# Kernel tuning notes

Hardware: AMD Instinct MI355X
Metric: run time of the kernel (lower is better)

Reference implementation:

```python
import jax, jax.numpy as jnp
import numpy as np

VOCAB, POS = 50000, 64
WDIM, PDIM = 256, 64
LSTM_H = 512          # total bidirectional width
H = LSTM_H // 2       # per-direction hidden
MLP = 512
SEQ = 512


def _lstm_dir(x, Wih, Whh, bih, bhh, reverse):
    # x: [T, in]; Wih: [4H, in]; Whh: [4H, H]; gate order i,f,g,o (PyTorch)
    Hd = Whh.shape[1]
    def step(carry, xt):
        h, c = carry
        g = xt @ Wih.T + bih + h @ Whh.T + bhh
        i, f, gg, o = jnp.split(g, 4, axis=-1)
        c = jax.nn.sigmoid(f) * c + jax.nn.sigmoid(i) * jnp.tanh(gg)
        h = jax.nn.sigmoid(o) * jnp.tanh(c)
        return (h, c), h
    xs = x[::-1] if reverse else x
    init = (jnp.zeros((Hd,), x.dtype), jnp.zeros((Hd,), x.dtype))
    _, hs = jax.lax.scan(step, init, xs)
    return hs[::-1] if reverse else hs


def _bilstm_layer(x, Wih, Whh, bih, bhh):
    # params stacked over direction: [2, ...]
    hf = _lstm_dir(x, Wih[0], Whh[0], bih[0], bhh[0], False)
    hb = _lstm_dir(x, Wih[1], Whh[1], bih[1], bhh[1], True)
    return jnp.concatenate([hf, hb], axis=-1)  # [T, 2H]


def setup_inputs() -> dict:
    key = jax.random.key(0)
    ks = jax.random.split(key, 16)
    s = 0.05
    inp = {
        "word_tensor": jax.random.randint(ks[0], (SEQ,), 0, VOCAB),
        "pos_tensor": jax.random.randint(ks[1], (SEQ,), 0, POS),
        "word_emb": jax.random.normal(ks[2], (VOCAB, WDIM), jnp.float32) * s,
        "pos_emb": jax.random.normal(ks[3], (POS, PDIM), jnp.float32) * s,
        # layer 0: input = WDIM+PDIM = 320
        "wih0": jax.random.normal(ks[4], (2, 4 * H, WDIM + PDIM), jnp.float32) * s,
        "whh0": jax.random.normal(ks[5], (2, 4 * H, H), jnp.float32) * s,
        "bih0": jax.random.normal(ks[6], (2, 4 * H), jnp.float32) * s,
        "bhh0": jax.random.normal(ks[7], (2, 4 * H), jnp.float32) * s,
        # layer 1: input = 2H = LSTM_H
        "wih1": jax.random.normal(ks[8], (2, 4 * H, LSTM_H), jnp.float32) * s,
        "whh1": jax.random.normal(ks[9], (2, 4 * H, H), jnp.float32) * s,
        "bih1": jax.random.normal(ks[10], (2, 4 * H), jnp.float32) * s,
        "bhh1": jax.random.normal(ks[11], (2, 4 * H), jnp.float32) * s,
        # pairwise MLP: Linear(2*LSTM_H -> MLP), output_layer(MLP -> 1)
        "W_lin": jax.random.normal(ks[12], (MLP, 2 * LSTM_H), jnp.float32) * s,
        "b_lin": jax.random.normal(ks[13], (MLP,), jnp.float32) * s,
        "w_out": jax.random.normal(ks[14], (1, MLP), jnp.float32) * s,
        "b_out": jax.random.normal(ks[15], (1,), jnp.float32) * s,
    }
    return inp


def reference(word_tensor, pos_tensor, word_emb, pos_emb,
              wih0, whh0, bih0, bhh0, wih1, whh1, bih1, bhh1,
              W_lin, b_lin, w_out, b_out):
    # embeddings: [T, 320]
    embeds = jnp.concatenate([word_emb[word_tensor], pos_emb[pos_tensor]], axis=-1)
    x = _bilstm_layer(embeds, wih0, whh0, bih0, bhh0)
    lstm_out = _bilstm_layer(x, wih1, whh1, bih1, bhh1)  # [T, LSTM_H]
    # Fused pairwise scoring: Linear(cat(h_h, h_m)) = h_h @ W1.T + h_m @ W2.T + b
    W1, W2 = W_lin[:, :LSTM_H], W_lin[:, LSTM_H:]
    u = lstm_out @ W1.T  # [T, MLP] head half
    v = lstm_out @ W2.T  # [T, MLP] modifier half
    neuron = jnp.tanh(u[:, None, :] + v[None, :, :] + b_lin)  # [T, T, MLP]
    score = neuron @ w_out[0] + b_out[0]                      # [T, T]
    n = score.shape[0]
    # original puts NaN on the diagonal (invalid h==m pairs); use 0.0 sentinel
    return jnp.where(jnp.eye(n, dtype=bool), 0.0, score)
```

## Files before the change

### kernel.cpp

```cpp
#include <hip/hip_runtime.h>
#include <cstddef>
#include <cstdint>

constexpr int kSeq = 512;
constexpr int kH   = 256;
constexpr int kG   = 1024;
constexpr int kE   = 320;
constexpr int kLH  = 512;
constexpr int kMLP = 512;

typedef _Float16 h2 __attribute__((ext_vector_type(2)));

__device__ __forceinline__ float fexp2f(float x) {
  float r; asm("v_exp_f32 %0, %1" : "=v"(r) : "v"(x)); return r;
}
__device__ __forceinline__ float frcpf(float x) {
  float r; asm("v_rcp_f32 %0, %1" : "=v"(r) : "v"(x)); return r;
}
__device__ __forceinline__ float sigm(float x) {
  return frcpf(1.0f + fexp2f(-1.4426950408889634f * x));
}
__device__ __forceinline__ float tanh_(float x) {
  return 1.0f - 2.0f * frcpf(1.0f + fexp2f(2.8853900817779268f * x));
}

__device__ __forceinline__ float fdot2(unsigned int w, unsigned int h, float c) {
#if __has_builtin(__builtin_amdgcn_fdot2)
  return __builtin_amdgcn_fdot2(__builtin_bit_cast(h2, w),
                                __builtin_bit_cast(h2, h), c, false);
#else
  const h2 wv = __builtin_bit_cast(h2, w);
  const h2 hv = __builtin_bit_cast(h2, h);
  return c + (float)wv.x * (float)hv.x + (float)wv.y * (float)hv.y;
#endif
}

__device__ __forceinline__ unsigned int packh2(float a, float b) {
  h2 v; v.x = (_Float16)a; v.y = (_Float16)b;
  return __builtin_bit_cast(unsigned int, v);
}

__global__ void embed_k(const int* __restrict__ wt, const int* __restrict__ pt,
                        const float* __restrict__ we, const float* __restrict__ pe,
                        float* __restrict__ X) {
  const int t = blockIdx.x;
  const int c = threadIdx.x;
  const int w = wt[t];
  const int p = pt[t];
  X[t * kE + c] = (c < 256) ? we[(size_t)w * 256 + c] : pe[p * 64 + (c - 256)];
}

__global__ __launch_bounds__(256) void pack_wh_k(
    const float* __restrict__ whh0, const float* __restrict__ whh1,
    unsigned int* __restrict__ wh16) {
  const int idx = blockIdx.x * 256 + threadIdx.x;
  const int layer = idx >> 18;
  const int li = idx & 262143;
  const int rowg = li >> 7;
  const int c2 = li & 127;
  const float* src = (layer ? whh1 : whh0) + (size_t)rowg * kH + c2 * 2;
  wh16[idx] = packh2(src[0], src[1]);
}

template <int BM, int BN, int BK>
__global__ __launch_bounds__(256) void gemm_nt(
    const float* __restrict__ A, int lda,
    const float* __restrict__ B, int ldb,
    const float* __restrict__ b1, const float* __restrict__ b2, float scale,
    float* __restrict__ C, int csm, int csn, int K) {
  const int tid = threadIdx.x;
  const int m0 = blockIdx.y * BM;
  const int n0 = blockIdx.x * BN;
  __shared__ float As[BK][BM];
  __shared__ float Bs[BK][BN];
  const int lm = tid >> 2;
  const int lk = tid & 3;
  const int tx = tid & 15;
  const int ty = tid >> 4;
  float acc[4][4] = {};
  for (int k0 = 0; k0 < K; k0 += BK) {
    const float4 av = *(const float4*)(A + (size_t)(m0 + lm) * lda + k0 + lk * 4);
    const float4 bv = *(const float4*)(B + (size_t)(n0 + lm) * ldb + k0 + lk * 4);
    __syncthreads();
    As[lk * 4 + 0][lm] = av.x; As[lk * 4 + 1][lm] = av.y;
    As[lk * 4 + 2][lm] = av.z; As[lk * 4 + 3][lm] = av.w;
    Bs[lk * 4 + 0][lm] = bv.x; Bs[lk * 4 + 1][lm] = bv.y;
    Bs[lk * 4 + 2][lm] = bv.z; Bs[lk * 4 + 3][lm] = bv.w;
    __syncthreads();
#pragma unroll
    for (int kk = 0; kk < BK; ++kk) {
      const float4 a = *(const float4*)&As[kk][ty * 4];
      const float4 b = *(const float4*)&Bs[kk][tx * 4];
      acc[0][0] = fmaf(a.x, b.x, acc[0][0]);
      acc[0][1] = fmaf(a.x, b.y, acc[0][1]);
      acc[0][2] = fmaf(a.x, b.z, acc[0][2]);
      acc[0][3] = fmaf(a.x, b.w, acc[0][3]);
      acc[1][0] = fmaf(a.y, b.x, acc[1][0]);
      acc[1][1] = fmaf(a.y, b.y, acc[1][1]);
      acc[1][2] = fmaf(a.y, b.z, acc[1][2]);
      acc[1][3] = fmaf(a.y, b.w, acc[1][3]);
      acc[2][0] = fmaf(a.z, b.x, acc[2][0]);
      acc[2][1] = fmaf(a.z, b.y, acc[2][1]);
      acc[2][2] = fmaf(a.z, b.z, acc[2][2]);
      acc[2][3] = fmaf(a.z, b.w, acc[2][3]);
      acc[3][0] = fmaf(a.w, b.x, acc[3][0]);
      acc[3][1] = fmaf(a.w, b.y, acc[3][1]);
      acc[3][2] = fmaf(a.w, b.z, acc[3][2]);
      acc[3][3] = fmaf(a.w, b.w, acc[3][3]);
    }
  }
#pragma unroll
  for (int ii = 0; ii < 4; ++ii) {
#pragma unroll
    for (int jj = 0; jj < 4; ++jj) {
      const int m = m0 + ty * 4 + ii;
      const int n = n0 + tx * 4 + jj;
      float v = acc[ii][jj];
      if (b1) v += b1[n];
      if (b2) v += b2[n];
      C[(size_t)m * csm + (size_t)n * csn] = v * scale;
    }
  }
}

__global__ __launch_bounds__(1024)
__attribute__((amdgpu_waves_per_eu(4, 4)))
void lstm_scan_2cu(
    const unsigned int* __restrict__ wh16,
    const float* __restrict__ pre,
    float* __restrict__ out,
    float* __restrict__ comm)
{
  const int bx = blockIdx.x;
  int d, s;
  if (bx == 0)      { d = 0; s = 0; }
  else if (bx == 1) { d = 1; s = 0; }
  else if (bx == 8) { d = 0; s = 1; }
  else if (bx == 9) { d = 1; s = 1; }
  else return;

  const int t = threadIdx.x;
  const int w = t >> 6;
  const int L = t & 63;
  const int ch = w & 1;
  const int r  = (w >> 1) * 64 + L;
  const int g  = r >> 7;
  const int j  = r & 127;
  const int grow = g * kH + s * 128 + j;

  uint4 wr[16];
  {
    const uint4* wp = (const uint4*)wh16 + ((size_t)d * kG + grow) * 32 + ch * 16;
#pragma unroll
    for (int k = 0; k < 16; ++k) wr[k] = wp[k];
  }

  __shared__ __align__(16) _Float16 hh16[kH];
  __shared__ float pbuf[2][512];
  if (t < 128) ((h2*)hh16)[t] = h2{(_Float16)0.f, (_Float16)0.f};
  float c = 0.0f;
  __syncthreads();

  const uint4* hh4 = (const uint4*)hh16;
  float* cm = comm + (size_t)d * kSeq * kH;
  const bool isGate = (t < 128);
  const bool isPoll = (t >= 512 && t < 640);
  const int re = (1 - s) * 128 + (t - 512);

  for (int u = 0; u < kSeq; ++u) {
    const int ts = d ? (kSeq - 1 - u) : u;
    float pg0 = 0.f, pg1 = 0.f, pg2 = 0.f, pg3 = 0.f;
    if (isGate) {
      const float* pp = pre + ((size_t)d * kSeq + ts) * kG + s * 128 + t;
      pg0 = pp[0]; pg1 = pp[256]; pg2 = pp[512]; pg3 = pp[768];
    }
    {
      const uint4* hp = hh4 + ch * 16;
      float a0 = 0.f, a1 = 0.f, a2 = 0.f, a3 = 0.f;
#pragma unroll
      for (int k = 0; k < 16; ++k) {
        const uint4 hv = hp[k];
        a0 = fdot2(wr[k].x, hv.x, a0);
        a1 = fdot2(wr[k].y, hv.y, a1);
        a2 = fdot2(wr[k].z, hv.z, a2);
        a3 = fdot2(wr[k].w, hv.w, a3);
      }
      pbuf[ch][r] = (a0 + a1) + (a2 + a3);
    }
    __syncthreads();

    if (isGate) {
      const float gi = pbuf[0][t]       + pbuf[1][t]       + pg0;
      const float gf = pbuf[0][128 + t] + pbuf[1][128 + t] + pg1;
      const float gg = pbuf[0][256 + t] + pbuf[1][256 + t] + pg2;
      const float go = pbuf[0][384 + t] + pbuf[1][384 + t] + pg3;
      const float iv = sigm(gi), fv = sigm(gf);
      const float gv = tanh_(gg), ov = sigm(go);
      c = fv * c + iv * gv;
      const float h = ov * tanh_(c);
      const int e = s * 128 + t;
      __hip_atomic_store(&cm[(size_t)u * kH + e], h + 2.0f,
                         __ATOMIC_RELAXED, __HIP_MEMORY_SCOPE_AGENT);
      hh16[e] = (_Float16)h;
      out[(size_t)ts * kLH + d * kH + e] = h;
    } else if (isPoll) {
      const float* src = &cm[(size_t)u * kH + re];
      float a = __hip_atomic_load(src, __ATOMIC_RELAXED, __HIP_MEMORY_SCOPE_AGENT);
      float b = __hip_atomic_load(src, __ATOMIC_RELAXED, __HIP_MEMORY_SCOPE_AGENT);
      while (a == 0.0f) {
        a = b;
        b = __hip_atomic_load(src, __ATOMIC_RELAXED, __HIP_MEMORY_SCOPE_AGENT);
      }
      hh16[re] = (_Float16)(a - 2.0f);
    }
    __syncthreads();
  }
}

__global__ __launch_bounds__(512) void score_k(
    const float* __restrict__ Up, const float* __restrict__ VT,
    const float* __restrict__ wout, const float* __restrict__ bout,
    float* __restrict__ out) {
  const int i = blockIdx.x;
  const int j = threadIdx.x;
  __shared__ float u_sh[kMLP];
  __shared__ float w_sh[kMLP];
  u_sh[j] = Up[(size_t)i * kMLP + j];
  w_sh[j] = wout[j];
  __syncthreads();
  float acc = 0.0f;
#pragma unroll 4
  for (int m = 0; m < kMLP; ++m) {
    const float x = u_sh[m] + VT[(size_t)m * kSeq + j];
    const float th = 1.0f - 2.0f * frcpf(1.0f + fexp2f(x));
    acc = fmaf(th, w_sh[m], acc);
  }
  const float s = acc + bout[0];
  out[(size_t)i * kSeq + j] = (j == i) ? 0.0f : s;
}

extern "C" void kernel_launch(void* const* d_in, const int* in_sizes, int n_in,
                              void* d_out, int out_size, void* d_ws, size_t ws_size,
                              hipStream_t stream) {
  const int*   wt   = (const int*)d_in[0];
  const int*   pt   = (const int*)d_in[1];
  const float* wemb = (const float*)d_in[2];
  const float* pemb = (const float*)d_in[3];
  const float* wih0 = (const float*)d_in[4];
  const float* whh0 = (const float*)d_in[5];
  const float* bih0 = (const float*)d_in[6];
  const float* bhh0 = (const float*)d_in[7];
  const float* wih1 = (const float*)d_in[8];
  const float* whh1 = (const float*)d_in[9];
  const float* bih1 = (const float*)d_in[10];
  const float* bhh1 = (const float*)d_in[11];
  const float* wlin = (const float*)d_in[12];
  const float* blin = (const float*)d_in[13];
  const float* wout = (const float*)d_in[14];
  const float* bout = (const float*)d_in[15];
  float* outp = (float*)d_out;

  float* ws   = (float*)d_ws;
  float* X    = ws;
  float* PG0  = X + kSeq * kE;
  float* X1   = PG0 + 2 * kSeq * kG;
  float* PG1  = X1 + kSeq * kLH;
  float* LOUT = PG1 + 2 * kSeq * kG;
  float* U    = LOUT + kSeq * kLH;
  float* VT   = U + kSeq * kMLP;
  float* COMM0 = VT + kSeq * kMLP;
  float* COMM1 = COMM0 + 2 * kSeq * kH;
  unsigned int* WH16 = (unsigned int*)(COMM1 + 2 * kSeq * kH);

  const float SC = 2.8853900817779268f;

  hipMemsetAsync(COMM0, 0, 2 * 2 * kSeq * kH * sizeof(float), stream);

  embed_k<<<kSeq, kE, 0, stream>>>(wt, pt, wemb, pemb, X);
  pack_wh_k<<<2048, 256, 0, stream>>>(whh0, whh1, WH16);

  for (int d = 0; d < 2; ++d) {
    gemm_nt<64, 64, 16><<<dim3(kG / 64, kSeq / 64), 256, 0, stream>>>(
        X, kE, wih0 + (size_t)d * kG * kE, kE,
        bih0 + d * kG, bhh0 + d * kG, 1.0f,
        PG0 + (size_t)d * kSeq * kG, kG, 1, kE);
  }
  lstm_scan_2cu<<<10, 1024, 0, stream>>>(WH16, PG0, X1, COMM0);

  for (int d = 0; d < 2; ++d) {
    gemm_nt<64, 64, 16><<<dim3(kG / 64, kSeq / 64), 256, 0, stream>>>(
        X1, kLH, wih1 + (size_t)d * kG * kLH, kLH,
        bih1 + d * kG, bhh1 + d * kG, 1.0f,
        PG1 + (size_t)d * kSeq * kG, kG, 1, kLH);
  }
  lstm_scan_2cu<<<10, 1024, 0, stream>>>(WH16 + 2 * kG * 128, PG1, LOUT, COMM1);

  gemm_nt<64, 64, 16><<<dim3(kMLP / 64, kSeq / 64), 256, 0, stream>>>(
      LOUT, kLH, wlin, 2 * kLH, nullptr, nullptr, SC,
      U, kMLP, 1, kLH);
  gemm_nt<64, 64, 16><<<dim3(kMLP / 64, kSeq / 64), 256, 0, stream>>>(
      LOUT, kLH, wlin + kLH, 2 * kLH, blin, nullptr, SC,
      VT, 1, kSeq, kLH);

  score_k<<<kSeq, 512, 0, stream>>>(U, VT, wout, bout, outp);
}
```

Measured before the change: 1.626 ms.

## Overlap local-half recurrent dot product with remote hidden-state polling

Each block's waves handling the locally produced half of h now compute their partial dot product right after the gate waves signal completion via a shared-memory counter. Before, this work waited for the next barrier. The partial sum now overlaps the cross-block poll for the remote half, which takes work off the serial recurrence critical path. Gate and poll roles are reassigned to whole waves so they don't conflict. This adds intra-block spin-waiting on an LDS atomic and more complex role logic.

```diff
diff --git a/kernel.cpp b/kernel.cpp
--- a/kernel.cpp
+++ b/kernel.cpp
@@ -157,24 +157,29 @@
 
   __shared__ __align__(16) _Float16 hh16[kH];
   __shared__ float pbuf[2][512];
+  __shared__ unsigned int gflag;
+  ((float*)pbuf)[t] = 0.0f;
   if (t < 128) ((h2*)hh16)[t] = h2{(_Float16)0.f, (_Float16)0.f};
+  if (t == 0) gflag = 0u;
   float c = 0.0f;
   __syncthreads();
 
   const uint4* hh4 = (const uint4*)hh16;
   float* cm = comm + (size_t)d * kSeq * kH;
-  const bool isGate = (t < 128);
-  const bool isPoll = (t >= 512 && t < 640);
-  const int re = (1 - s) * 128 + (t - 512);
+  const bool isGateWave = (w < 2);
+  const int pw0 = 8 + (1 - s);
+  const int pw1 = 10 + (1 - s);
+  const bool isPoll = (w == pw0) || (w == pw1);
+  const int re = (1 - s) * 128 + ((w == pw1) ? 64 : 0) + L;
 
   for (int u = 0; u < kSeq; ++u) {
     const int ts = d ? (kSeq - 1 - u) : u;
     float pg0 = 0.f, pg1 = 0.f, pg2 = 0.f, pg3 = 0.f;
-    if (isGate) {
+    if (isGateWave) {
       const float* pp = pre + ((size_t)d * kSeq + ts) * kG + s * 128 + t;
       pg0 = pp[0]; pg1 = pp[256]; pg2 = pp[512]; pg3 = pp[768];
     }
-    {
+    if (ch != s) {
       const uint4* hp = hh4 + ch * 16;
       float a0 = 0.f, a1 = 0.f, a2 = 0.f, a3 = 0.f;
 #pragma unroll
@@ -189,7 +194,7 @@
     }
     __syncthreads();
 
-    if (isGate) {
+    if (isGateWave) {
       const float gi = pbuf[0][t]       + pbuf[1][t]       + pg0;
       const float gf = pbuf[0][128 + t] + pbuf[1][128 + t] + pg1;
       const float gg = pbuf[0][256 + t] + pbuf[1][256 + t] + pg2;
@@ -203,6 +208,9 @@
                          __ATOMIC_RELAXED, __HIP_MEMORY_SCOPE_AGENT);
       hh16[e] = (_Float16)h;
       out[(size_t)ts * kLH + d * kH + e] = h;
+      if (L == 0)
+        __hip_atomic_fetch_add(&gflag, 1u, __ATOMIC_RELEASE,
+                               __HIP_MEMORY_SCOPE_WORKGROUP);
     } else if (isPoll) {
       const float* src = &cm[(size_t)u * kH + re];
       float a = __hip_atomic_load(src, __ATOMIC_RELAXED, __HIP_MEMORY_SCOPE_AGENT);
@@ -212,6 +220,22 @@
         b = __hip_atomic_load(src, __ATOMIC_RELAXED, __HIP_MEMORY_SCOPE_AGENT);
       }
       hh16[re] = (_Float16)(a - 2.0f);
+    }
+    if (ch == s) {
+      const unsigned int want = 2u * (unsigned)(u + 1);
+      while (__hip_atomic_load(&gflag, __ATOMIC_ACQUIRE,
+                               __HIP_MEMORY_SCOPE_WORKGROUP) < want) {}
+      const uint4* hp = hh4 + ch * 16;
+      float a0 = 0.f, a1 = 0.f, a2 = 0.f, a3 = 0.f;
+#pragma unroll
+      for (int k = 0; k < 16; ++k) {
+        const uint4 hv = hp[k];
+        a0 = fdot2(wr[k].x, hv.x, a0);
+        a1 = fdot2(wr[k].y, hv.y, a1);
+        a2 = fdot2(wr[k].z, hv.z, a2);
+        a3 = fdot2(wr[k].w, hv.w, a3);
+      }
+      pbuf[ch][r] = (a0 + a1) + (a2 + a3);
     }
     __syncthreads();
   }
```

Result: slower. 1.891 ms (+16.3%).
